# Kernel optimization log

Measured on AMD Instinct MI355X. Metric: run time of the kernel, lower is better.

The kernel has to match this reference:

```python
import jax, jax.numpy as jnp
import numpy as np

D, J, K, H = 4, 256, 512, 512  # d, num_output, num_input, num_hidden
B = 1024


def setup_inputs() -> dict:
    key = jax.random.key(0)
    ks = jax.random.split(key, 8)
    x = jax.random.normal(ks[0], (B, K), dtype=jnp.float32)
    # self.w = ((1-0.1)*U + 0.1) / num_input, shape [d, num_output, num_input]
    w = ((0.9 * jax.random.uniform(ks[1], (D, J, K), dtype=jnp.float32) + 0.1) / K)
    # Stacked per-output-MLP params (nn.Linear default init scale 1/sqrt(fan_in))
    s0 = 1.0 / np.sqrt(K)
    s1 = 1.0 / np.sqrt(H)
    W0 = jax.random.uniform(ks[2], (J, H, K), dtype=jnp.float32, minval=-s0, maxval=s0)
    b0 = jax.random.uniform(ks[3], (J, H), dtype=jnp.float32, minval=-s0, maxval=s0)
    W1 = jax.random.uniform(ks[4], (J, H), dtype=jnp.float32, minval=-s1, maxval=s1)  # [J,1,H] squeezed
    b1 = jax.random.uniform(ks[5], (J,), dtype=jnp.float32, minval=-s1, maxval=s1)
    logvar = jnp.ones((D,), dtype=jnp.float32) * -4.0
    return {"x": x, "i": 0, "w": w, "W0": W0, "b0": b0, "W1": W1, "b1": b1, "logvar": logvar}


def reference(x, i, w, W0, b0, W1, b1, logvar):
    # For each output j: mu[:, j] = lin1_j(LeakyReLU(lin0_j(w[i, j] * x)))
    # Fused as a single grouped GEMM over j: fold the mask w[i] into the contraction.
    wi = w[i]                                   # [J, K]
    h = jnp.einsum('jhk,jk,bk->bjh', W0, wi, x) + b0[None, :, :]   # [B, J, H]
    h = jax.nn.leaky_relu(h, negative_slope=0.01)
    mu = jnp.einsum('bjh,jh->bj', h, W1) + b1[None, :]             # [B, J]
    return (mu, logvar)
```

## Files before the change

kernel.cpp:

```cpp
#include <hip/hip_runtime.h>

#define J_ 256
#define K_ 512
#define H_ 512
#define B_ 1024
#define BK 64

typedef float f32x4 __attribute__((ext_vector_type(4)));
typedef unsigned int u32x4 __attribute__((ext_vector_type(4)));
typedef unsigned short u16x4 __attribute__((ext_vector_type(4)));
typedef unsigned short u16x8 __attribute__((ext_vector_type(8)));
typedef __bf16 bf16x8 __attribute__((ext_vector_type(8)));

__device__ __forceinline__ unsigned short f2bf(float f) {
    unsigned int u = __float_as_uint(f);
    u += 0x7fffu + ((u >> 16) & 1u);
    return (unsigned short)(u >> 16);
}

__device__ __forceinline__ void gload_lds16(const void* g, void* l) {
    __builtin_amdgcn_global_load_lds(
        (const __attribute__((address_space(1))) unsigned int*)g,
        (__attribute__((address_space(3))) unsigned int*)l, 16, 0, 0);
}

__global__ __launch_bounds__(256) void prep_kernel(
    const float* __restrict__ x, const float* __restrict__ b1,
    const float* __restrict__ logvar, unsigned short* __restrict__ xbf,
    float* __restrict__ out) {
    int t = blockIdx.x * 256 + threadIdx.x;
    {
        f32x4 v = *(const f32x4*)(x + (size_t)t * 4);
        u16x4 o;
        o[0] = f2bf(v[0]); o[1] = f2bf(v[1]); o[2] = f2bf(v[2]); o[3] = f2bf(v[3]);
        *(u16x4*)(xbf + (size_t)t * 4) = o;
    }
    if (t < (B_ * J_) / 4) {
        int b = t >> 6;
        int j4 = (t & 63) << 2;
        f32x4 bb = *(const f32x4*)(b1 + j4);
        *(f32x4*)(out + ((size_t)b << 8) + j4) = bb;
    }
    if (t < 4) out[B_ * J_ + t] = logvar[t];
}

__global__ __launch_bounds__(256) void wprep_kernel(
    const float* __restrict__ W0, const float* __restrict__ wmask,
    const int* __restrict__ ip, unsigned short* __restrict__ w0p) {
    size_t t = (size_t)blockIdx.x * 256 + threadIdx.x;
    size_t e = t * 8;
    int j = (int)(e >> 18);
    int k = (int)(e & (K_ - 1));
    const float* wi = wmask + ((size_t)ip[0] * J_ + j) * K_ + k;
    f32x4 s0 = *(const f32x4*)wi;
    f32x4 s1 = *(const f32x4*)(wi + 4);
    f32x4 a0 = *(const f32x4*)(W0 + e);
    f32x4 a1 = *(const f32x4*)(W0 + e + 4);
    a0 *= s0; a1 *= s1;
    u16x8 o;
    #pragma unroll
    for (int q = 0; q < 4; ++q) { o[q] = f2bf(a0[q]); o[q + 4] = f2bf(a1[q]); }
    *(u16x8*)(w0p + e) = o;
}

__global__ __launch_bounds__(256, 3) void enc_kernel(
    const unsigned short* __restrict__ xbf,
    const unsigned short* __restrict__ w0p,
    const float* __restrict__ b0,
    const float* __restrict__ W1,
    float* __restrict__ out) {
    __shared__ unsigned char ldsA[128 * 128];
    __shared__ unsigned char ldsB[128 * 128];

    int p = blockIdx.x;
    int xcd = p & 7;
    int q = p >> 3;
    int j = (xcd << 5) + (q >> 5);
    int inner = q & 31;
    int m0 = (inner >> 2) << 7;
    int h0 = (inner & 3) << 7;

    int tid = threadIdx.x;
    int lane = tid & 63;
    int wv = tid >> 6;
    int wm = wv >> 1, wn = wv & 1;
    int lr = lane & 15, lg = lane >> 4;
    int lrow = lane >> 3;
    int lch = lane & 7;
    int sch = ((lch ^ lrow) << 3);

    const unsigned short* aBase = xbf + (size_t)(m0 + wv * 32 + lrow) * K_ + sch;
    const unsigned short* bBase = w0p + ((size_t)j * H_ + h0 + wv * 32 + lrow) * K_ + sch;
    unsigned char* laBase = ldsA + wv * 4096;
    unsigned char* lbBase = ldsB + wv * 4096;

    f32x4 acc[4][4] = {};

    for (int ks = 0; ks < K_ / BK; ++ks) {
        int k0 = ks * BK;
        #pragma unroll
        for (int ii = 0; ii < 4; ++ii) {
            gload_lds16(aBase + (size_t)ii * 8 * K_ + k0, laBase + ii * 1024);
            gload_lds16(bBase + (size_t)ii * 8 * K_ + k0, lbBase + ii * 1024);
        }
        __syncthreads();
        #pragma unroll
        for (int kf = 0; kf < 2; ++kf) {
            bf16x8 af[4], bfr[4];
            #pragma unroll
            for (int mf = 0; mf < 4; ++mf) {
                int r = (wm << 6) + (mf << 4) + lr;
                af[mf] = *(const bf16x8*)(ldsA + r * 128 +
                          (((kf << 6) + (lg << 4)) ^ ((r & 7) << 4)));
            }
            #pragma unroll
            for (int nf = 0; nf < 4; ++nf) {
                int hrw = (wn << 6) + (nf << 4) + lr;
                bfr[nf] = *(const bf16x8*)(ldsB + hrw * 128 +
                          (((kf << 6) + (lg << 4)) ^ ((hrw & 7) << 4)));
            }
            #pragma unroll
            for (int mf = 0; mf < 4; ++mf)
                #pragma unroll
                for (int nf = 0; nf < 4; ++nf)
                    acc[mf][nf] = __builtin_amdgcn_mfma_f32_16x16x32_bf16(
                        af[mf], bfr[nf], acc[mf][nf], 0, 0, 0);
        }
        __syncthreads();
    }

    float b0v[4], w1v[4];
    #pragma unroll
    for (int nf = 0; nf < 4; ++nf) {
        int h = h0 + (wn << 6) + (nf << 4) + lr;
        b0v[nf] = b0[(size_t)j * H_ + h];
        w1v[nf] = W1[(size_t)j * H_ + h];
    }
    #pragma unroll
    for (int mf = 0; mf < 4; ++mf) {
        #pragma unroll
        for (int rg = 0; rg < 4; ++rg) {
            float ps = 0.f;
            #pragma unroll
            for (int nf = 0; nf < 4; ++nf) {
                float hv = acc[mf][nf][rg] + b0v[nf];
                hv = hv > 0.f ? hv : 0.01f * hv;
                ps += hv * w1v[nf];
            }
            ps += __shfl_xor(ps, 1);
            ps += __shfl_xor(ps, 2);
            ps += __shfl_xor(ps, 4);
            ps += __shfl_xor(ps, 8);
            if (lr == 0) {
                int row = m0 + (wm << 6) + (mf << 4) + (lg << 2) + rg;
                atomicAdd(out + (size_t)row * J_ + j, ps);
            }
        }
    }
}

__global__ __launch_bounds__(256, 2) void enc_kernel_fb(
    const unsigned short* __restrict__ xbf,
    const float* __restrict__ W0,
    const float* __restrict__ wmask,
    const int* __restrict__ ip,
    const float* __restrict__ b0,
    const float* __restrict__ W1,
    float* __restrict__ out) {
    __shared__ unsigned char ldsA[128 * 128];
    __shared__ unsigned char ldsB[128 * 128];

    int p = blockIdx.x;
    int xcd = p & 7;
    int q = p >> 3;
    int j = (xcd << 5) + (q >> 5);
    int inner = q & 31;
    int m0 = (inner >> 2) << 7;
    int h0 = (inner & 3) << 7;

    int i = ip[0];
    const float* w0j = W0 + (size_t)j * (H_ * K_);
    const float* wij = wmask + ((size_t)i * J_ + j) * K_;

    int tid = threadIdx.x;
    int lane = tid & 63;
    int wv = tid >> 6;
    int wm = wv >> 1, wn = wv & 1;
    int lr = lane & 15, lg = lane >> 4;
    int srow0 = tid >> 3;
    int c = tid & 7;

    f32x4 acc[4][4] = {};

    for (int ks = 0; ks < K_ / BK; ++ks) {
        int k0 = ks * BK;
        #pragma unroll
        for (int it = 0; it < 4; ++it) {
            int r = srow0 + it * 32;
            u32x4 v = *(const u32x4*)(xbf + (size_t)(m0 + r) * K_ + k0 + c * 8);
            *(u32x4*)(ldsA + r * 128 + ((c * 16) ^ ((r & 7) << 4))) = v;
        }
        f32x4 s0 = *(const f32x4*)(wij + k0 + c * 8);
        f32x4 s1 = *(const f32x4*)(wij + k0 + c * 8 + 4);
        #pragma unroll
        for (int it = 0; it < 4; ++it) {
            int hr = srow0 + it * 32;
            const float* src = w0j + (size_t)(h0 + hr) * K_ + k0 + c * 8;
            f32x4 a0 = *(const f32x4*)(src);
            f32x4 a1 = *(const f32x4*)(src + 4);
            a0 *= s0; a1 *= s1;
            u16x8 bv;
            #pragma unroll
            for (int e = 0; e < 4; ++e) { bv[e] = f2bf(a0[e]); bv[e + 4] = f2bf(a1[e]); }
            *(u16x8*)(ldsB + hr * 128 + ((c * 16) ^ ((hr & 7) << 4))) = bv;
        }
        __syncthreads();
        #pragma unroll
        for (int kf = 0; kf < 2; ++kf) {
            bf16x8 af[4], bfr[4];
            #pragma unroll
            for (int mf = 0; mf < 4; ++mf) {
                int r = (wm << 6) + (mf << 4) + lr;
                af[mf] = *(const bf16x8*)(ldsA + r * 128 +
                          (((kf << 6) + (lg << 4)) ^ ((r & 7) << 4)));
            }
            #pragma unroll
            for (int nf = 0; nf < 4; ++nf) {
                int hrw = (wn << 6) + (nf << 4) + lr;
                bfr[nf] = *(const bf16x8*)(ldsB + hrw * 128 +
                          (((kf << 6) + (lg << 4)) ^ ((hrw & 7) << 4)));
            }
            #pragma unroll
            for (int mf = 0; mf < 4; ++mf)
                #pragma unroll
                for (int nf = 0; nf < 4; ++nf)
                    acc[mf][nf] = __builtin_amdgcn_mfma_f32_16x16x32_bf16(
                        af[mf], bfr[nf], acc[mf][nf], 0, 0, 0);
        }
        __syncthreads();
    }

    float b0v[4], w1v[4];
    #pragma unroll
    for (int nf = 0; nf < 4; ++nf) {
        int h = h0 + (wn << 6) + (nf << 4) + lr;
        b0v[nf] = b0[(size_t)j * H_ + h];
        w1v[nf] = W1[(size_t)j * H_ + h];
    }
    #pragma unroll
    for (int mf = 0; mf < 4; ++mf) {
        #pragma unroll
        for (int rg = 0; rg < 4; ++rg) {
            float ps = 0.f;
            #pragma unroll
            for (int nf = 0; nf < 4; ++nf) {
                float hv = acc[mf][nf][rg] + b0v[nf];
                hv = hv > 0.f ? hv : 0.01f * hv;
                ps += hv * w1v[nf];
            }
            ps += __shfl_xor(ps, 1);
            ps += __shfl_xor(ps, 2);
            ps += __shfl_xor(ps, 4);
            ps += __shfl_xor(ps, 8);
            if (lr == 0) {
                int row = m0 + (wm << 6) + (mf << 4) + (lg << 2) + rg;
                atomicAdd(out + (size_t)row * J_ + j, ps);
            }
        }
    }
}

extern "C" void kernel_launch(void* const* d_in, const int* in_sizes, int n_in,
                              void* d_out, int out_size, void* d_ws, size_t ws_size,
                              hipStream_t stream) {
    const float* x      = (const float*)d_in[0];
    const int*   ip     = (const int*)d_in[1];
    const float* wmask  = (const float*)d_in[2];
    const float* W0     = (const float*)d_in[3];
    const float* b0     = (const float*)d_in[4];
    const float* W1     = (const float*)d_in[5];
    const float* b1     = (const float*)d_in[6];
    const float* logvar = (const float*)d_in[7];
    float* out = (float*)d_out;
    unsigned short* xbf = (unsigned short*)d_ws;
    const size_t xbf_elems = (size_t)B_ * K_;
    const size_t w0p_bytes = (size_t)J_ * H_ * K_ * 2;
    const size_t need = xbf_elems * 2 + w0p_bytes;

    prep_kernel<<<512, 256, 0, stream>>>(x, b1, logvar, xbf, out);
    if (ws_size >= need) {
        unsigned short* w0p = xbf + xbf_elems;
        wprep_kernel<<<32768, 256, 0, stream>>>(W0, wmask, ip, w0p);
        enc_kernel<<<8192, 256, 0, stream>>>(xbf, w0p, b0, W1, out);
    } else {
        enc_kernel_fb<<<8192, 256, 0, stream>>>(xbf, W0, wmask, ip, b0, W1, out);
    }
}
```

Before: 582.4 us.

## Triple-buffer LDS with async global-to-LDS loads and larger 256x128 tiles

Rewrites the main grouped-GEMM kernel to use 512-thread blocks computing 256x128 tiles, with a three-stage LDS ring buffer filled by global_load_lds. Loads are issued two stages ahead and tracked with explicit vmcnt waits and raw barriers. MFMA sections get raised wave priority via setprio. The goal is to overlap global memory latency with matrix compute and halve the number of blocks and atomics. In exchange it uses 144KB of LDS, so only one block fits per CU, and it relies on hand-counted vmcnt values being correct.

```diff
diff --git a/kernel.cpp b/kernel.cpp
--- a/kernel.cpp
+++ b/kernel.cpp
@@ -4,7 +4,6 @@
 #define K_ 512
 #define H_ 512
 #define B_ 1024
-#define BK 64
 
 typedef float f32x4 __attribute__((ext_vector_type(4)));
 typedef unsigned int u32x4 __attribute__((ext_vector_type(4)));
@@ -63,78 +62,92 @@
     *(u16x8*)(w0p + e) = o;
 }
 
-__global__ __launch_bounds__(256, 3) void enc_kernel(
+__global__ __launch_bounds__(512, 1) void enc_kernel(
     const unsigned short* __restrict__ xbf,
     const unsigned short* __restrict__ w0p,
     const float* __restrict__ b0,
     const float* __restrict__ W1,
     float* __restrict__ out) {
-    __shared__ unsigned char ldsA[128 * 128];
-    __shared__ unsigned char ldsB[128 * 128];
+    __shared__ unsigned char lds[3 * 49152];
 
     int p = blockIdx.x;
     int xcd = p & 7;
     int q = p >> 3;
-    int j = (xcd << 5) + (q >> 5);
-    int inner = q & 31;
-    int m0 = (inner >> 2) << 7;
+    int j = (xcd << 5) + (q >> 4);
+    int inner = q & 15;
+    int m0 = (inner >> 2) << 8;
     int h0 = (inner & 3) << 7;
 
     int tid = threadIdx.x;
     int lane = tid & 63;
     int wv = tid >> 6;
-    int wm = wv >> 1, wn = wv & 1;
+    int wmv = wv >> 1;
+    int wnv = wv & 1;
     int lr = lane & 15, lg = lane >> 4;
+
     int lrow = lane >> 3;
     int lch = lane & 7;
     int sch = ((lch ^ lrow) << 3);
 
-    const unsigned short* aBase = xbf + (size_t)(m0 + wv * 32 + lrow) * K_ + sch;
-    const unsigned short* bBase = w0p + ((size_t)j * H_ + h0 + wv * 32 + lrow) * K_ + sch;
-    unsigned char* laBase = ldsA + wv * 4096;
-    unsigned char* lbBase = ldsB + wv * 4096;
+    const unsigned short* aSrc = xbf + (size_t)(m0 + wv * 8 + lrow) * K_ + sch;
+    const unsigned short* bSrc = w0p + ((size_t)j * H_ + h0 + wv * 8 + lrow) * K_ + sch;
+    unsigned char* ldsAW = lds + wv * 1024;
+    unsigned char* ldsBW = lds + 32768 + wv * 1024;
 
     f32x4 acc[4][4] = {};
 
-    for (int ks = 0; ks < K_ / BK; ++ks) {
-        int k0 = ks * BK;
-        #pragma unroll
-        for (int ii = 0; ii < 4; ++ii) {
-            gload_lds16(aBase + (size_t)ii * 8 * K_ + k0, laBase + ii * 1024);
-            gload_lds16(bBase + (size_t)ii * 8 * K_ + k0, lbBase + ii * 1024);
-        }
-        __syncthreads();
-        #pragma unroll
-        for (int kf = 0; kf < 2; ++kf) {
-            bf16x8 af[4], bfr[4];
-            #pragma unroll
-            for (int mf = 0; mf < 4; ++mf) {
-                int r = (wm << 6) + (mf << 4) + lr;
-                af[mf] = *(const bf16x8*)(ldsA + r * 128 +
-                          (((kf << 6) + (lg << 4)) ^ ((r & 7) << 4)));
-            }
-            #pragma unroll
-            for (int nf = 0; nf < 4; ++nf) {
-                int hrw = (wn << 6) + (nf << 4) + lr;
-                bfr[nf] = *(const bf16x8*)(ldsB + hrw * 128 +
-                          (((kf << 6) + (lg << 4)) ^ ((hrw & 7) << 4)));
-            }
-            #pragma unroll
-            for (int mf = 0; mf < 4; ++mf)
-                #pragma unroll
-                for (int nf = 0; nf < 4; ++nf)
-                    acc[mf][nf] = __builtin_amdgcn_mfma_f32_16x16x32_bf16(
-                        af[mf], bfr[nf], acc[mf][nf], 0, 0, 0);
-        }
-        __syncthreads();
-    }
+#define VMW(n) do { asm volatile("s_waitcnt vmcnt(" #n ")" ::: "memory"); \
+                    __builtin_amdgcn_sched_barrier(0); } while (0)
+#define BAR() do { __builtin_amdgcn_s_barrier(); \
+                   __builtin_amdgcn_sched_barrier(0); } while (0)
+
+#define STAGE(bi, ks) do { \
+    _Pragma("unroll") for (int ii = 0; ii < 4; ++ii) \
+        gload_lds16(aSrc + (size_t)ii * 64 * K_ + (ks) * 64, \
+                    ldsAW + (bi) * 49152 + ii * 8192); \
+    _Pragma("unroll") for (int ii = 0; ii < 2; ++ii) \
+        gload_lds16(bSrc + (size_t)ii * 64 * K_ + (ks) * 64, \
+                    ldsBW + (bi) * 49152 + ii * 8192); \
+    } while (0)
+
+#define COMPUTE(bi) do { \
+    const unsigned char* LA = lds + (bi) * 49152; \
+    const unsigned char* LB = LA + 32768; \
+    _Pragma("unroll") for (int kf = 0; kf < 2; ++kf) { \
+        bf16x8 af[4], bv[4]; \
+        int colk = (kf << 6) + (lg << 4); \
+        _Pragma("unroll") for (int mf = 0; mf < 4; ++mf) { \
+            int r = (wmv << 6) + (mf << 4) + lr; \
+            af[mf] = *(const bf16x8*)(LA + r * 128 + (colk ^ ((r & 7) << 4))); \
+        } \
+        _Pragma("unroll") for (int nf = 0; nf < 4; ++nf) { \
+            int hr = (wnv << 6) + (nf << 4) + lr; \
+            bv[nf] = *(const bf16x8*)(LB + hr * 128 + (colk ^ ((hr & 7) << 4))); \
+        } \
+        __builtin_amdgcn_s_setprio(1); \
+        _Pragma("unroll") for (int mf = 0; mf < 4; ++mf) \
+            _Pragma("unroll") for (int nf = 0; nf < 4; ++nf) \
+                acc[mf][nf] = __builtin_amdgcn_mfma_f32_16x16x32_bf16( \
+                    af[mf], bv[nf], acc[mf][nf], 0, 0, 0); \
+        __builtin_amdgcn_s_setprio(0); \
+    } } while (0)
+
+    STAGE(0, 0); STAGE(1, 1);
+    STAGE(2, 2); VMW(12); BAR(); COMPUTE(0); BAR();
+    STAGE(0, 3); VMW(12); BAR(); COMPUTE(1); BAR();
+    STAGE(1, 4); VMW(12); BAR(); COMPUTE(2); BAR();
+    STAGE(2, 5); VMW(12); BAR(); COMPUTE(0); BAR();
+    STAGE(0, 6); VMW(12); BAR(); COMPUTE(1); BAR();
+    STAGE(1, 7); VMW(12); BAR(); COMPUTE(2); BAR();
+                 VMW(6);  BAR(); COMPUTE(0); BAR();
+                 VMW(0);  BAR(); COMPUTE(1);
 
     float b0v[4], w1v[4];
     #pragma unroll
     for (int nf = 0; nf < 4; ++nf) {
-        int h = h0 + (wn << 6) + (nf << 4) + lr;
-        b0v[nf] = b0[(size_t)j * H_ + h];
-        w1v[nf] = W1[(size_t)j * H_ + h];
+        int col = h0 + (wnv << 6) + (nf << 4) + lr;
+        b0v[nf] = b0[(size_t)j * H_ + col];
+        w1v[nf] = W1[(size_t)j * H_ + col];
     }
     #pragma unroll
     for (int mf = 0; mf < 4; ++mf) {
@@ -152,11 +165,15 @@
             ps += __shfl_xor(ps, 4);
             ps += __shfl_xor(ps, 8);
             if (lr == 0) {
-                int row = m0 + (wm << 6) + (mf << 4) + (lg << 2) + rg;
+                int row = m0 + (wmv << 6) + (mf << 4) + (lg << 2) + rg;
                 atomicAdd(out + (size_t)row * J_ + j, ps);
             }
         }
     }
+#undef VMW
+#undef BAR
+#undef STAGE
+#undef COMPUTE
 }
 
 __global__ __launch_bounds__(256, 2) void enc_kernel_fb(
@@ -192,8 +209,8 @@
 
     f32x4 acc[4][4] = {};
 
-    for (int ks = 0; ks < K_ / BK; ++ks) {
-        int k0 = ks * BK;
+    for (int ks = 0; ks < K_ / 64; ++ks) {
+        int k0 = ks * 64;
         #pragma unroll
         for (int it = 0; it < 4; ++it) {
             int r = srow0 + it * 32;
@@ -209,10 +226,10 @@
             f32x4 a0 = *(const f32x4*)(src);
             f32x4 a1 = *(const f32x4*)(src + 4);
             a0 *= s0; a1 *= s1;
-            u16x8 bv;
-            #pragma unroll
-            for (int e = 0; e < 4; ++e) { bv[e] = f2bf(a0[e]); bv[e + 4] = f2bf(a1[e]); }
-            *(u16x8*)(ldsB + hr * 128 + ((c * 16) ^ ((hr & 7) << 4))) = bv;
+            u16x8 bvv;
+            #pragma unroll
+            for (int e = 0; e < 4; ++e) { bvv[e] = f2bf(a0[e]); bvv[e + 4] = f2bf(a1[e]); }
+            *(u16x8*)(ldsB + hr * 128 + ((c * 16) ^ ((hr & 7) << 4))) = bvv;
         }
         __syncthreads();
         #pragma unroll
@@ -291,7 +308,7 @@
     if (ws_size >= need) {
         unsigned short* w0p = xbf + xbf_elems;
         wprep_kernel<<<32768, 256, 0, stream>>>(W0, wmask, ip, w0p);
-        enc_kernel<<<8192, 256, 0, stream>>>(xbf, w0p, b0, W1, out);
+        enc_kernel<<<4096, 512, 0, stream>>>(xbf, w0p, b0, W1, out);
     } else {
         enc_kernel_fb<<<8192, 256, 0, stream>>>(xbf, W0, wmask, ip, b0, W1, out);
     }
```

New measurement: 587.0 us. Within noise of the previous version (+0.8%).
